# Kernel optimization log

Measured on AMD Instinct MI355X. Metric: run time of the kernel, lower is better.

Reference implementation:

```python
import jax, jax.numpy as jnp
import numpy as np

B, L, D, H, FF = 8, 512, 1024, 16, 1024
HD = D // H
EPS = 1e-5
ROPE_BASE = 10000.0
ROPE_DIM = D  # module passes dim=embed_dim (not head_dim) to RotaryPositionalEmbeddings


def _layer_norm(x, g, b):
    m = jnp.mean(x, axis=-1, keepdims=True)
    v = jnp.var(x, axis=-1, keepdims=True)
    return (x - m) * jax.lax.rsqrt(v + EPS) * g + b


def _rope(x):
    # x: [B, H, L, HD]; interleaved-pair rotation, frequencies base**(-2i/ROPE_DIM)
    half = HD // 2
    inv_freq = 1.0 / (ROPE_BASE ** (jnp.arange(half, dtype=jnp.float32) * 2.0 / ROPE_DIM))
    ang = jnp.arange(L, dtype=jnp.float32)[:, None] * inv_freq[None, :]  # [L, half]
    cos = jnp.cos(ang)
    sin = jnp.sin(ang)
    xr = x.reshape(*x.shape[:-1], half, 2)
    x1, x2 = xr[..., 0], xr[..., 1]
    out = jnp.stack([x1 * cos - x2 * sin, x1 * sin + x2 * cos], axis=-1)
    return out.reshape(x.shape).astype(x.dtype)


def setup_inputs() -> dict:
    key = jax.random.key(0)
    ks = jax.random.split(key, 16)
    sd = 0.02
    n = lambda k, shape: (jax.random.normal(k, shape, dtype=jnp.float32) * sd)
    return {
        "input_ids": jax.random.normal(ks[0], (B, L, D), dtype=jnp.float32),
        "Wq": n(ks[1], (FF, D)), "bq": jnp.zeros((D,), jnp.float32),
        "Wk": n(ks[2], (FF, D)), "bk": jnp.zeros((D,), jnp.float32),
        "Wv": n(ks[3], (FF, D)), "bv": jnp.zeros((D,), jnp.float32),
        "Wo": n(ks[4], (D, D)),  "bo": jnp.zeros((D,), jnp.float32),
        "Wf": n(ks[5], (D, FF)), "bf": jnp.zeros((FF,), jnp.float32),
        "g_ffn": jnp.ones((D,), jnp.float32), "b_ffn": jnp.zeros((D,), jnp.float32),
        "g_attn": jnp.ones((FF,), jnp.float32), "b_attn": jnp.zeros((FF,), jnp.float32),
    }


def reference(input_ids, Wq, bq, Wk, bk, Wv, bv, Wo, bo, Wf, bf,
              g_ffn, b_ffn, g_attn, b_attn):
    # FFN branch: computed then DISCARDED in the original source (x is overwritten).
    _ffn_dead = jax.nn.relu(_layer_norm(input_ids, g_ffn, b_ffn) @ Wf + bf)  # noqa: F841

    x = _layer_norm(input_ids, g_attn, b_attn)  # pre_attn_norm applied to input_ids
    q = (x @ Wq + bq).reshape(B, L, H, HD).transpose(0, 2, 1, 3)  # [B,H,L,HD]
    k = (x @ Wk + bk).reshape(B, L, H, HD).transpose(0, 2, 1, 3)
    v = (x @ Wv + bv).reshape(B, L, H, HD).transpose(0, 2, 1, 3)
    q = _rope(q)
    k = _rope(k)

    scale = 1.0 / np.sqrt(HD).astype(np.float32)
    scores = jnp.einsum("bhqd,bhkd->bhqk", q, k) * scale  # [B,H,L,L]
    attn = jax.nn.softmax(scores, axis=-1)
    o = jnp.einsum("bhqk,bhkd->bhqd", attn, v)
    o = o.transpose(0, 2, 1, 3).reshape(B, L, D)
    return input_ids + (o @ Wo + bo)
```

## Files before the change

kernel.cpp:

```cpp
#include <hip/hip_runtime.h>

typedef unsigned short ushort_t;
typedef short bf16x8 __attribute__((ext_vector_type(8)));
typedef float f32x4 __attribute__((ext_vector_type(4)));

#define B_ 8
#define L_ 512
#define D_ 1024
#define H_ 16
#define M_ 4096

__device__ __forceinline__ ushort_t f2bf(float f) {
  union { float f; unsigned u; } v; v.f = f;
  unsigned r = v.u + 0x7FFFu + ((v.u >> 16) & 1u);
  return (ushort_t)(r >> 16);
}

__device__ __forceinline__ void gl_lds16(const ushort_t* g, ushort_t* s) {
  __builtin_amdgcn_global_load_lds((const __attribute__((address_space(1))) void*)(g),
                                   (__attribute__((address_space(3))) void*)(s), 16, 0, 0);
}

__global__ __launch_bounds__(256) void prep_kernel(const float* __restrict__ x,
                                                   const float* __restrict__ g,
                                                   const float* __restrict__ b,
                                                   ushort_t* __restrict__ xn,
                                                   float2* __restrict__ csb,
                                                   const float* __restrict__ w0,
                                                   const float* __restrict__ w1,
                                                   const float* __restrict__ w2,
                                                   const float* __restrict__ w3,
                                                   ushort_t* __restrict__ wt) {
  __shared__ float red[8];
  __shared__ float tile[32][33];
  int blk = blockIdx.x, t = threadIdx.x;
  if (blk < 4096) {
    int row = blk;
    float4 v = ((const float4*)(x + (size_t)row * D_))[t];
    float s  = v.x + v.y + v.z + v.w;
    float s2 = v.x * v.x + v.y * v.y + v.z * v.z + v.w * v.w;
#pragma unroll
    for (int m = 1; m < 64; m <<= 1) { s += __shfl_xor(s, m); s2 += __shfl_xor(s2, m); }
    int w = t >> 6;
    if ((t & 63) == 0) { red[w] = s; red[4 + w] = s2; }
    __syncthreads();
    s  = red[0] + red[1] + red[2] + red[3];
    s2 = red[4] + red[5] + red[6] + red[7];
    float mean = s * (1.0f / D_);
    float var  = s2 * (1.0f / D_) - mean * mean;
    float rs   = rsqrtf(var + 1e-5f);
    float4 gg = ((const float4*)g)[t];
    float4 bb = ((const float4*)b)[t];
    unsigned long long pk =
        (unsigned long long)f2bf((v.x - mean) * rs * gg.x + bb.x)
      | ((unsigned long long)f2bf((v.y - mean) * rs * gg.y + bb.y) << 16)
      | ((unsigned long long)f2bf((v.z - mean) * rs * gg.z + bb.z) << 32)
      | ((unsigned long long)f2bf((v.w - mean) * rs * gg.w + bb.w) << 48);
    *(unsigned long long*)(xn + (size_t)row * D_ + t * 4) = pk;
  } else if (blk < 4160) {
    int idx = (blk - 4096) * 256 + t;
    int l = idx >> 5, i = idx & 31;
    float inv = powf(10000.0f, (-2.0f * (float)i) / 1024.0f);
    float ang = (float)l * inv;
    csb[idx] = make_float2(cosf(ang), sinf(ang));
  } else {
    int wb = blk - 4160;
    int z = wb >> 10;
    const float* W = (z == 0) ? w0 : (z == 1) ? w1 : (z == 2) ? w2 : w3;
    ushort_t* WT = wt + ((size_t)z << 20);
    int rem = wb & 1023;
    int by = rem >> 5, bx = rem & 31;
    int tx = t & 31, ty = t >> 5;
    int k0 = by * 32, n0 = bx * 32;
#pragma unroll
    for (int j = 0; j < 4; ++j)
      tile[ty + 8 * j][tx] = W[(size_t)(k0 + ty + 8 * j) * 1024 + n0 + tx];
    __syncthreads();
#pragma unroll
    for (int j = 0; j < 4; ++j)
      WT[(size_t)(n0 + ty + 8 * j) * 1024 + k0 + tx] = f2bf(tile[tx][ty + 8 * j]);
  }
}

__global__ __launch_bounds__(256) void gemm_qkv_kernel(const ushort_t* __restrict__ xn,
                                                       const ushort_t* __restrict__ wt,
                                                       const float* __restrict__ bq,
                                                       const float* __restrict__ bk,
                                                       const float* __restrict__ bv,
                                                       ushort_t* __restrict__ qb,
                                                       ushort_t* __restrict__ kb,
                                                       ushort_t* __restrict__ vt,
                                                       const float2* __restrict__ csb) {
  __shared__ ushort_t As[64 * 64];
  __shared__ ushort_t Bs[128 * 64];
  int t = threadIdx.x, l = t & 63, w = t >> 6, lr = l & 15, lg = l >> 4;
  int hid = blockIdx.x;
  int xcd = hid & 7, lid = hid >> 3;
  int by = (xcd >> 1) * 16 + lid / 12;
  int bx = (xcd & 1) * 12 + lid % 12;
  int m0 = by * 64;
  int n0g = bx * 128;
  int z = n0g >> 10;
  int n0 = n0g & 1023;
  const float* bias = (z == 0) ? bq : (z == 1) ? bk : bv;
  int wr = w >> 1, wc = w & 1;
  const int sr8 = l >> 3;
  const int scol = ((l & 7) ^ sr8) * 8;

  f32x4 acc[2][4] = {};

  for (int k0 = 0; k0 < 1024; k0 += 64) {
    gl_lds16(&xn[(size_t)(m0 + w * 16 + sr8) * 1024 + k0 + scol], &As[(w * 16) * 64]);
    gl_lds16(&xn[(size_t)(m0 + w * 16 + 8 + sr8) * 1024 + k0 + scol], &As[(w * 16 + 8) * 64]);
    gl_lds16(&wt[(size_t)(n0g + w * 32 + sr8) * 1024 + k0 + scol], &Bs[(w * 32) * 64]);
    gl_lds16(&wt[(size_t)(n0g + w * 32 + 8 + sr8) * 1024 + k0 + scol], &Bs[(w * 32 + 8) * 64]);
    gl_lds16(&wt[(size_t)(n0g + w * 32 + 16 + sr8) * 1024 + k0 + scol], &Bs[(w * 32 + 16) * 64]);
    gl_lds16(&wt[(size_t)(n0g + w * 32 + 24 + sr8) * 1024 + k0 + scol], &Bs[(w * 32 + 24) * 64]);
    __syncthreads();
#pragma unroll
    for (int kk = 0; kk < 2; ++kk) {
      bf16x8 a[2], bfr[4];
#pragma unroll
      for (int mi = 0; mi < 2; ++mi)
        a[mi] = *(const bf16x8*)&As[(wr * 32 + mi * 16 + lr) * 64 + (((kk * 4 + lg) ^ (lr & 7)) << 3)];
#pragma unroll
      for (int ni = 0; ni < 4; ++ni)
        bfr[ni] = *(const bf16x8*)&Bs[(wc * 64 + ni * 16 + lr) * 64 + (((kk * 4 + lg) ^ (lr & 7)) << 3)];
#pragma unroll
      for (int mi = 0; mi < 2; ++mi)
#pragma unroll
        for (int ni = 0; ni < 4; ++ni)
          acc[mi][ni] = __builtin_amdgcn_mfma_f32_16x16x32_bf16(a[mi], bfr[ni], acc[mi][ni], 0, 0, 0);
    }
    __syncthreads();
  }

  if (z < 2) {
    ushort_t* outp = (z == 0) ? qb : kb;
    const float sc = (z == 0) ? 0.125f : 1.0f;
#pragma unroll
    for (int mi = 0; mi < 2; ++mi) {
      int rowb = m0 + wr * 32 + mi * 16 + lg * 4;
#pragma unroll
      for (int ni = 0; ni < 4; ++ni) {
        int col = n0 + wc * 64 + ni * 16 + lr;
        float bvv = bias[col];
        int ii = (col & 63) >> 1;
        int codd = col & 1;
#pragma unroll
        for (int r = 0; r < 4; ++r) {
          float val = acc[mi][ni][r] + bvv;
          float par = __shfl_xor(val, 1);
          float2 cs = csb[((rowb + r) & 511) * 32 + ii];
          float y = codd ? (par * cs.y + val * cs.x) : (val * cs.x - par * cs.y);
          outp[(size_t)(rowb + r) * 1024 + col] = f2bf(y * sc);
        }
      }
    }
  } else {
#pragma unroll
    for (int mi = 0; mi < 2; ++mi) {
      int rowb = m0 + wr * 32 + mi * 16 + lg * 4;
      int bidx = rowb >> 9, l0 = rowb & 511;
#pragma unroll
      for (int ni = 0; ni < 4; ++ni) {
        int col = n0 + wc * 64 + ni * 16 + lr;
        float bvv = bias[col];
        unsigned long long pk =
            (unsigned long long)f2bf(acc[mi][ni][0] + bvv)
          | ((unsigned long long)f2bf(acc[mi][ni][1] + bvv) << 16)
          | ((unsigned long long)f2bf(acc[mi][ni][2] + bvv) << 32)
          | ((unsigned long long)f2bf(acc[mi][ni][3] + bvv) << 48);
        *(unsigned long long*)&vt[((size_t)(bidx << 10) + col) * 512 + l0] = pk;
      }
    }
  }
}

__global__ __launch_bounds__(256) void gemm_o_kernel(const ushort_t* __restrict__ A,
                                                     const ushort_t* __restrict__ Bt,
                                                     const float* __restrict__ bias,
                                                     const float* __restrict__ res,
                                                     float* __restrict__ out) {
  __shared__ ushort_t As[64 * 64];
  __shared__ ushort_t Bs[128 * 64];
  int t = threadIdx.x, l = t & 63, w = t >> 6, lr = l & 15, lg = l >> 4;
  int hid = blockIdx.x;
  int lid = (hid & 7) * 64 + (hid >> 3);
  int bx = lid & 7, by = lid >> 3;
  int m0 = by * 64, n0 = bx * 128;
  int wr = w >> 1, wc = w & 1;
  const int srow = l >> 3;
  const int scol = ((l & 7) ^ (srow & 7)) * 8;

  f32x4 acc[2][4] = {};

  for (int k0 = 0; k0 < 1024; k0 += 64) {
#pragma unroll
    for (int i = 0; i < 2; ++i)
      gl_lds16(&A[(size_t)(m0 + w * 16 + i * 8 + srow) * 1024 + k0 + scol],
               &As[(w * 16 + i * 8) * 64]);
#pragma unroll
    for (int i = 0; i < 4; ++i)
      gl_lds16(&Bt[(size_t)(n0 + w * 32 + i * 8 + srow) * 1024 + k0 + scol],
               &Bs[(w * 32 + i * 8) * 64]);
    __syncthreads();
#pragma unroll
    for (int kk = 0; kk < 2; ++kk) {
      bf16x8 a[2], bfr[4];
#pragma unroll
      for (int mi = 0; mi < 2; ++mi)
        a[mi] = *(const bf16x8*)&As[(wr * 32 + mi * 16 + lr) * 64 + (((kk * 4 + lg) ^ (lr & 7)) << 3)];
#pragma unroll
      for (int ni = 0; ni < 4; ++ni)
        bfr[ni] = *(const bf16x8*)&Bs[(wc * 64 + ni * 16 + lr) * 64 + (((kk * 4 + lg) ^ (lr & 7)) << 3)];
#pragma unroll
      for (int mi = 0; mi < 2; ++mi)
#pragma unroll
        for (int ni = 0; ni < 4; ++ni)
          acc[mi][ni] = __builtin_amdgcn_mfma_f32_16x16x32_bf16(a[mi], bfr[ni], acc[mi][ni], 0, 0, 0);
    }
    __syncthreads();
  }

#pragma unroll
  for (int mi = 0; mi < 2; ++mi) {
    int rowb = m0 + wr * 32 + mi * 16 + lg * 4;
#pragma unroll
    for (int ni = 0; ni < 4; ++ni) {
      int col = n0 + wc * 64 + ni * 16 + lr;
      float bvv = bias[col];
#pragma unroll
      for (int r = 0; r < 4; ++r) {
        size_t off = (size_t)(rowb + r) * 1024 + col;
        out[off] = acc[mi][ni][r] + bvv + res[off];
      }
    }
  }
}

__global__ __launch_bounds__(256) void attn_kernel(const ushort_t* __restrict__ q,
                                                   const ushort_t* __restrict__ k,
                                                   const ushort_t* __restrict__ vt,
                                                   ushort_t* __restrict__ o) {
  __shared__ ushort_t Ks[2][64 * 64];
  __shared__ ushort_t Vs[2][64 * 64];
  __shared__ ushort_t Ps[4][2][16 * 64];
  int t = threadIdx.x, l = t & 63, w = t >> 6, lr = l & 15, lg = l >> 4;
  int blk = blockIdx.x;
  int bh = blk & 127, qt = blk >> 7;
  int b = bh >> 4, h = bh & 15;
  const int srow = l >> 3;
  const int scol = ((l & 7) ^ (srow & 7)) * 8;

  bf16x8 qf[2][2];
#pragma unroll
  for (int qm = 0; qm < 2; ++qm) {
    size_t qrow = (size_t)(b * 512 + qt * 128 + w * 32 + qm * 16 + lr);
#pragma unroll
    for (int kh = 0; kh < 2; ++kh)
      qf[qm][kh] = *(const bf16x8*)&q[qrow * 1024 + h * 64 + kh * 32 + lg * 8];
  }

  f32x4 oacc[2][4] = {};
  float mrun[2] = {-1e30f, -1e30f};
  float lrun[2] = {0.f, 0.f};

#define STAGE(buf, kv0)                                                              \
  {                                                                                  \
    _Pragma("unroll")                                                                \
    for (int j = 0; j < 2; ++j) {                                                    \
      gl_lds16(&k[(size_t)(b * 512 + (kv0) + w * 16 + j * 8 + srow) * 1024 + h * 64 + scol], \
               &Ks[buf][(w * 16 + j * 8) * 64]);                                     \
      gl_lds16(&vt[((size_t)bh * 64 + w * 16 + j * 8 + srow) * 512 + (kv0) + scol],  \
               &Vs[buf][(w * 16 + j * 8) * 64]);                                     \
    }                                                                                \
  }

  STAGE(0, 0);
  __syncthreads();
  int cur = 0;
  for (int it = 0; it < 8; ++it) {
    if (it < 7) { STAGE(cur ^ 1, (it + 1) * 64); }
    bf16x8 kf[2][4];
#pragma unroll
    for (int kh = 0; kh < 2; ++kh)
#pragma unroll
      for (int kn = 0; kn < 4; ++kn)
        kf[kh][kn] = *(const bf16x8*)&Ks[cur][(kn * 16 + lr) * 64 + (((kh * 4 + lg) ^ (lr & 7)) << 3)];

#pragma unroll
    for (int qm = 0; qm < 2; ++qm) {
      f32x4 st[4] = {};
#pragma unroll
      for (int kh = 0; kh < 2; ++kh)
#pragma unroll
        for (int kn = 0; kn < 4; ++kn)
          st[kn] = __builtin_amdgcn_mfma_f32_16x16x32_bf16(kf[kh][kn], qf[qm][kh], st[kn], 0, 0, 0);
      float mx = st[0][0];
#pragma unroll
      for (int kn = 0; kn < 4; ++kn)
#pragma unroll
        for (int r = 0; r < 4; ++r) mx = fmaxf(mx, st[kn][r]);
      mx = fmaxf(mx, __shfl_xor(mx, 16));
      mx = fmaxf(mx, __shfl_xor(mx, 32));
      float mn = mrun[qm], al = 1.0f;
      if (!__all(mx <= mrun[qm] + 8.0f)) {
        mn = fmaxf(mrun[qm], mx);
        al = __expf(mrun[qm] - mn);
        mrun[qm] = mn;
#pragma unroll
        for (int f = 0; f < 4; ++f) {
          oacc[qm][f][0] *= al; oacc[qm][f][1] *= al;
          oacc[qm][f][2] *= al; oacc[qm][f][3] *= al;
        }
      }
      float sm = 0.f;
#pragma unroll
      for (int kn = 0; kn < 4; ++kn) {
        float p0 = __expf(st[kn][0] - mn);
        float p1 = __expf(st[kn][1] - mn);
        float p2 = __expf(st[kn][2] - mn);
        float p3 = __expf(st[kn][3] - mn);
        sm += p0 + p1 + p2 + p3;
        int kvb = kn * 16 + 4 * lg;
        unsigned long long pk =
            (unsigned long long)f2bf(p0)
          | ((unsigned long long)f2bf(p1) << 16)
          | ((unsigned long long)f2bf(p2) << 32)
          | ((unsigned long long)f2bf(p3) << 48);
        *(unsigned long long*)&Ps[w][qm][lr * 64 + (((kvb >> 3) ^ (lr & 7)) << 3) + (kvb & 7)] = pk;
      }
      sm += __shfl_xor(sm, 16);
      sm += __shfl_xor(sm, 32);
      lrun[qm] = lrun[qm] * al + sm;
    }
    asm volatile("s_waitcnt lgkmcnt(0)" ::: "memory");
    __builtin_amdgcn_sched_barrier(0);
#pragma unroll
    for (int kk = 0; kk < 2; ++kk) {
      int sl = (((kk * 4 + lg) ^ (lr & 7)) << 3);
      bf16x8 pb[2];
#pragma unroll
      for (int qm = 0; qm < 2; ++qm)
        pb[qm] = *(const bf16x8*)&Ps[w][qm][lr * 64 + sl];
#pragma unroll
      for (int f = 0; f < 4; ++f) {
        bf16x8 vf = *(const bf16x8*)&Vs[cur][(f * 16 + lr) * 64 + sl];
#pragma unroll
        for (int qm = 0; qm < 2; ++qm)
          oacc[qm][f] = __builtin_amdgcn_mfma_f32_16x16x32_bf16(vf, pb[qm], oacc[qm][f], 0, 0, 0);
      }
    }
    __syncthreads();
    cur ^= 1;
  }
#pragma unroll
  for (int qm = 0; qm < 2; ++qm) {
    float inv = 1.0f / lrun[qm];
    size_t qrow = (size_t)(b * 512 + qt * 128 + w * 32 + qm * 16 + lr);
#pragma unroll
    for (int f = 0; f < 4; ++f) {
      unsigned long long pk =
          (unsigned long long)f2bf(oacc[qm][f][0] * inv)
        | ((unsigned long long)f2bf(oacc[qm][f][1] * inv) << 16)
        | ((unsigned long long)f2bf(oacc[qm][f][2] * inv) << 32)
        | ((unsigned long long)f2bf(oacc[qm][f][3] * inv) << 48);
      *(unsigned long long*)&o[qrow * 1024 + h * 64 + f * 16 + 4 * lg] = pk;
    }
  }
#undef STAGE
}

extern "C" void kernel_launch(void* const* d_in, const int* in_sizes, int n_in,
                              void* d_out, int out_size, void* d_ws, size_t ws_size,
                              hipStream_t stream) {
  const float* input_ids = (const float*)d_in[0];
  const float* Wq = (const float*)d_in[1];
  const float* bq = (const float*)d_in[2];
  const float* Wk = (const float*)d_in[3];
  const float* bk = (const float*)d_in[4];
  const float* Wv = (const float*)d_in[5];
  const float* bv = (const float*)d_in[6];
  const float* Wo = (const float*)d_in[7];
  const float* bo = (const float*)d_in[8];
  const float* g_attn = (const float*)d_in[13];
  const float* b_attn = (const float*)d_in[14];
  float* out = (float*)d_out;

  char* ws = (char*)d_ws;
  const size_t MB = 1024 * 1024;
  ushort_t* wt = (ushort_t*)(ws);
  ushort_t* xn = (ushort_t*)(ws + 8 * MB);
  ushort_t* qb = (ushort_t*)(ws + 16 * MB);
  ushort_t* kb = (ushort_t*)(ws + 24 * MB);
  ushort_t* vt = (ushort_t*)(ws + 32 * MB);
  float2* csb  = (float2*)(ws + 40 * MB);

  prep_kernel<<<8256, 256, 0, stream>>>(input_ids, g_attn, b_attn, xn, csb,
                                        Wq, Wk, Wv, Wo, wt);
  gemm_qkv_kernel<<<1536, 256, 0, stream>>>(xn, wt, bq, bk, bv, qb, kb, vt, csb);
  attn_kernel<<<512, 256, 0, stream>>>(qb, kb, vt, xn);
  gemm_o_kernel<<<512, 256, 0, stream>>>(xn, wt + 3 * MB, bo, input_ids, out);
}
```

Measured before the change: 90.11 us.

## Shrink QKV GEMM tiles to 64x64 with two waves; one-wave-per-row layernorm

The QKV projection GEMM now uses 64x64 output tiles with 128 threads (two waves), doubling the grid to 3072 blocks so more blocks can be resident and tail effects shrink. The cost is lower arithmetic intensity, since each A tile is reused across only 64 columns. The layernorm part of the prep kernel now handles four rows per block, one wave per row, which removes the LDS reduction and the block barrier. That cuts the layernorm block count from 4096 to 1024.

```diff
diff --git a/kernel.cpp b/kernel.cpp
--- a/kernel.cpp
+++ b/kernel.cpp
@@ -31,40 +31,45 @@
                                                    const float* __restrict__ w2,
                                                    const float* __restrict__ w3,
                                                    ushort_t* __restrict__ wt) {
-  __shared__ float red[8];
   __shared__ float tile[32][33];
   int blk = blockIdx.x, t = threadIdx.x;
-  if (blk < 4096) {
-    int row = blk;
-    float4 v = ((const float4*)(x + (size_t)row * D_))[t];
-    float s  = v.x + v.y + v.z + v.w;
-    float s2 = v.x * v.x + v.y * v.y + v.z * v.z + v.w * v.w;
+  if (blk < 1024) {
+    int row = blk * 4 + (t >> 6);
+    int lane = t & 63;
+    const float4* xr = (const float4*)(x + (size_t)row * D_);
+    float4 v[4];
+    float s = 0.f, s2 = 0.f;
+#pragma unroll
+    for (int j = 0; j < 4; ++j) {
+      v[j] = xr[j * 64 + lane];
+      s  += v[j].x + v[j].y + v[j].z + v[j].w;
+      s2 += v[j].x * v[j].x + v[j].y * v[j].y + v[j].z * v[j].z + v[j].w * v[j].w;
+    }
 #pragma unroll
     for (int m = 1; m < 64; m <<= 1) { s += __shfl_xor(s, m); s2 += __shfl_xor(s2, m); }
-    int w = t >> 6;
-    if ((t & 63) == 0) { red[w] = s; red[4 + w] = s2; }
-    __syncthreads();
-    s  = red[0] + red[1] + red[2] + red[3];
-    s2 = red[4] + red[5] + red[6] + red[7];
     float mean = s * (1.0f / D_);
     float var  = s2 * (1.0f / D_) - mean * mean;
     float rs   = rsqrtf(var + 1e-5f);
-    float4 gg = ((const float4*)g)[t];
-    float4 bb = ((const float4*)b)[t];
-    unsigned long long pk =
-        (unsigned long long)f2bf((v.x - mean) * rs * gg.x + bb.x)
-      | ((unsigned long long)f2bf((v.y - mean) * rs * gg.y + bb.y) << 16)
-      | ((unsigned long long)f2bf((v.z - mean) * rs * gg.z + bb.z) << 32)
-      | ((unsigned long long)f2bf((v.w - mean) * rs * gg.w + bb.w) << 48);
-    *(unsigned long long*)(xn + (size_t)row * D_ + t * 4) = pk;
-  } else if (blk < 4160) {
-    int idx = (blk - 4096) * 256 + t;
+    unsigned long long* outp = (unsigned long long*)(xn + (size_t)row * D_);
+#pragma unroll
+    for (int j = 0; j < 4; ++j) {
+      float4 gg = ((const float4*)g)[j * 64 + lane];
+      float4 bb = ((const float4*)b)[j * 64 + lane];
+      unsigned long long pk =
+          (unsigned long long)f2bf((v[j].x - mean) * rs * gg.x + bb.x)
+        | ((unsigned long long)f2bf((v[j].y - mean) * rs * gg.y + bb.y) << 16)
+        | ((unsigned long long)f2bf((v[j].z - mean) * rs * gg.z + bb.z) << 32)
+        | ((unsigned long long)f2bf((v[j].w - mean) * rs * gg.w + bb.w) << 48);
+      outp[j * 64 + lane] = pk;
+    }
+  } else if (blk < 1088) {
+    int idx = (blk - 1024) * 256 + t;
     int l = idx >> 5, i = idx & 31;
     float inv = powf(10000.0f, (-2.0f * (float)i) / 1024.0f);
     float ang = (float)l * inv;
     csb[idx] = make_float2(cosf(ang), sinf(ang));
   } else {
-    int wb = blk - 4160;
+    int wb = blk - 1088;
     int z = wb >> 10;
     const float* W = (z == 0) ? w0 : (z == 1) ? w1 : (z == 2) ? w2 : w3;
     ushort_t* WT = wt + ((size_t)z << 20);
@@ -82,7 +87,7 @@
   }
 }
 
-__global__ __launch_bounds__(256) void gemm_qkv_kernel(const ushort_t* __restrict__ xn,
+__global__ __launch_bounds__(128) void gemm_qkv_kernel(const ushort_t* __restrict__ xn,
                                                        const ushort_t* __restrict__ wt,
                                                        const float* __restrict__ bq,
                                                        const float* __restrict__ bk,
@@ -92,40 +97,40 @@
                                                        ushort_t* __restrict__ vt,
                                                        const float2* __restrict__ csb) {
   __shared__ ushort_t As[64 * 64];
-  __shared__ ushort_t Bs[128 * 64];
+  __shared__ ushort_t Bs[64 * 64];
   int t = threadIdx.x, l = t & 63, w = t >> 6, lr = l & 15, lg = l >> 4;
   int hid = blockIdx.x;
   int xcd = hid & 7, lid = hid >> 3;
-  int by = (xcd >> 1) * 16 + lid / 12;
-  int bx = (xcd & 1) * 12 + lid % 12;
+  int by = (xcd >> 1) * 16 + lid / 24;
+  int bx = (xcd & 1) * 24 + lid % 24;
   int m0 = by * 64;
-  int n0g = bx * 128;
+  int n0g = bx * 64;
   int z = n0g >> 10;
   int n0 = n0g & 1023;
   const float* bias = (z == 0) ? bq : (z == 1) ? bk : bv;
-  int wr = w >> 1, wc = w & 1;
   const int sr8 = l >> 3;
   const int scol = ((l & 7) ^ sr8) * 8;
 
   f32x4 acc[2][4] = {};
 
   for (int k0 = 0; k0 < 1024; k0 += 64) {
-    gl_lds16(&xn[(size_t)(m0 + w * 16 + sr8) * 1024 + k0 + scol], &As[(w * 16) * 64]);
-    gl_lds16(&xn[(size_t)(m0 + w * 16 + 8 + sr8) * 1024 + k0 + scol], &As[(w * 16 + 8) * 64]);
-    gl_lds16(&wt[(size_t)(n0g + w * 32 + sr8) * 1024 + k0 + scol], &Bs[(w * 32) * 64]);
-    gl_lds16(&wt[(size_t)(n0g + w * 32 + 8 + sr8) * 1024 + k0 + scol], &Bs[(w * 32 + 8) * 64]);
-    gl_lds16(&wt[(size_t)(n0g + w * 32 + 16 + sr8) * 1024 + k0 + scol], &Bs[(w * 32 + 16) * 64]);
-    gl_lds16(&wt[(size_t)(n0g + w * 32 + 24 + sr8) * 1024 + k0 + scol], &Bs[(w * 32 + 24) * 64]);
+#pragma unroll
+    for (int i = 0; i < 4; ++i) {
+      gl_lds16(&xn[(size_t)(m0 + w * 32 + i * 8 + sr8) * 1024 + k0 + scol],
+               &As[(w * 32 + i * 8) * 64]);
+      gl_lds16(&wt[(size_t)(n0g + w * 32 + i * 8 + sr8) * 1024 + k0 + scol],
+               &Bs[(w * 32 + i * 8) * 64]);
+    }
     __syncthreads();
 #pragma unroll
     for (int kk = 0; kk < 2; ++kk) {
       bf16x8 a[2], bfr[4];
 #pragma unroll
       for (int mi = 0; mi < 2; ++mi)
-        a[mi] = *(const bf16x8*)&As[(wr * 32 + mi * 16 + lr) * 64 + (((kk * 4 + lg) ^ (lr & 7)) << 3)];
+        a[mi] = *(const bf16x8*)&As[(w * 32 + mi * 16 + lr) * 64 + (((kk * 4 + lg) ^ (lr & 7)) << 3)];
 #pragma unroll
       for (int ni = 0; ni < 4; ++ni)
-        bfr[ni] = *(const bf16x8*)&Bs[(wc * 64 + ni * 16 + lr) * 64 + (((kk * 4 + lg) ^ (lr & 7)) << 3)];
+        bfr[ni] = *(const bf16x8*)&Bs[(ni * 16 + lr) * 64 + (((kk * 4 + lg) ^ (lr & 7)) << 3)];
 #pragma unroll
       for (int mi = 0; mi < 2; ++mi)
 #pragma unroll
@@ -140,10 +145,10 @@
     const float sc = (z == 0) ? 0.125f : 1.0f;
 #pragma unroll
     for (int mi = 0; mi < 2; ++mi) {
-      int rowb = m0 + wr * 32 + mi * 16 + lg * 4;
+      int rowb = m0 + w * 32 + mi * 16 + lg * 4;
 #pragma unroll
       for (int ni = 0; ni < 4; ++ni) {
-        int col = n0 + wc * 64 + ni * 16 + lr;
+        int col = n0 + ni * 16 + lr;
         float bvv = bias[col];
         int ii = (col & 63) >> 1;
         int codd = col & 1;
@@ -160,11 +165,11 @@
   } else {
 #pragma unroll
     for (int mi = 0; mi < 2; ++mi) {
-      int rowb = m0 + wr * 32 + mi * 16 + lg * 4;
+      int rowb = m0 + w * 32 + mi * 16 + lg * 4;
       int bidx = rowb >> 9, l0 = rowb & 511;
 #pragma unroll
       for (int ni = 0; ni < 4; ++ni) {
-        int col = n0 + wc * 64 + ni * 16 + lr;
+        int col = n0 + ni * 16 + lr;
         float bvv = bias[col];
         unsigned long long pk =
             (unsigned long long)f2bf(acc[mi][ni][0] + bvv)
@@ -397,9 +402,9 @@
   ushort_t* vt = (ushort_t*)(ws + 32 * MB);
   float2* csb  = (float2*)(ws + 40 * MB);
 
-  prep_kernel<<<8256, 256, 0, stream>>>(input_ids, g_attn, b_attn, xn, csb,
+  prep_kernel<<<5184, 256, 0, stream>>>(input_ids, g_attn, b_attn, xn, csb,
                                         Wq, Wk, Wv, Wo, wt);
-  gemm_qkv_kernel<<<1536, 256, 0, stream>>>(xn, wt, bq, bk, bv, qb, kb, vt, csb);
+  gemm_qkv_kernel<<<3072, 128, 0, stream>>>(xn, wt, bq, bk, bv, qb, kb, vt, csb);
   attn_kernel<<<512, 256, 0, stream>>>(qb, kb, vt, xn);
   gemm_o_kernel<<<512, 256, 0, stream>>>(xn, wt + 3 * MB, bo, input_ids, out);
 }
```

Result: slower. 93.45 us (+3.7%).
